# Kernel optimization log

Measured on AMD Instinct MI355X. Metric: run time of the kernel, lower is better.

Reference implementation:

```python
import jax, jax.numpy as jnp
import numpy as np

NUM_STRINGS = 6
WEIGHT_FRET_ONSET = 0.5
STRING_WEIGHTS = jnp.ones((NUM_STRINGS,), dtype=jnp.float32)

B, S, T, C = 64, 6, 2000, 25


def setup_inputs() -> dict:
    key = jax.random.key(0)
    k1, k2, k3, k4 = jax.random.split(key, 4)
    return {
        "output_fret": jax.random.normal(k1, (B, S, T, C), dtype=jnp.float32),
        "target_fret": jax.random.randint(k2, (B, S, T), 0, C),
        "output_onset": jax.random.normal(k3, (B, S, T), dtype=jnp.float32),
        "target_onset": jax.random.uniform(k4, (B, S, T), dtype=jnp.float32),
    }


def reference(output_fret, target_fret, output_onset, target_onset):
    # ---- fret loss: standard CE over classes, mean over batch per (s,t),
    #      summed over frames, weighted per string ----
    logp_fret = jax.nn.log_softmax(output_fret, axis=-1)            # [B,S,T,C]
    nll = -jnp.take_along_axis(logp_fret, target_fret[..., None], axis=-1)[..., 0]  # [B,S,T]
    fret_st = nll.mean(axis=0)                                       # [S,T] (reduction='mean' over batch)
    fret_string_losses = fret_st.sum(axis=1) * STRING_WEIGHTS        # [S]
    fret_loss = fret_string_losses.sum()

    # ---- onset loss: torch CE with 1D [B] input + [B] float target =
    #      single example with B classes and probability targets:
    #      softmax over the BATCH dimension ----
    logp_on = jax.nn.log_softmax(output_onset, axis=0)               # softmax over B
    on_st = -(target_onset * logp_on).sum(axis=0)                    # [S,T]
    onset_string_losses = on_st.sum(axis=1) * STRING_WEIGHTS         # [S]
    onset_loss = onset_string_losses.sum()

    loss = WEIGHT_FRET_ONSET * fret_loss + (1.0 - WEIGHT_FRET_ONSET) * onset_loss
    return (loss, fret_loss, onset_loss, fret_string_losses, onset_string_losses)
```

## Files before the change

kernel.cpp:

```cpp
#include <hip/hip_runtime.h>
#include <math.h>

constexpr int Bn = 64, Sn = 6, Tn = 2000, Cn = 25;
constexpr int COLS = Sn * Tn;
constexpr int ROWS = Bn * Sn * Tn;
constexpr int BDIM = 256;
constexpr int RPB  = 256;
constexpr int FBLK = ROWS / RPB;
constexpr int FPAD = 3072;
constexpr int OBLK = (COLS + BDIM - 1) / BDIM;
constexpr int OPAD = 64;
constexpr int GRID = FBLK + OBLK;


__global__ __launch_bounds__(BDIM) void main_kernel(const float4* __restrict__ x4,
                                                    const int*    __restrict__ tgt,
                                                    const float*  __restrict__ ox,
                                                    const float*  __restrict__ ot,
                                                    float* __restrict__ pf,
                                                    float* __restrict__ po) {
    __shared__ float lds[RPB * Cn];
    __shared__ float ls[Sn];
    const int tid = threadIdx.x;
    if (tid < Sn) ls[tid] = 0.0f;

    if (blockIdx.x < OBLK) {
        __syncthreads();
        const int col = blockIdx.x * BDIM + tid;
        if (col < COLS) {
            float M = -INFINITY, S = 0.0f, ts = 0.0f, txs = 0.0f;
            for (int b0 = 0; b0 < Bn; b0 += 16) {
                float xv[16];
                #pragma unroll
                for (int k = 0; k < 16; ++k) xv[k] = ox[(b0 + k) * COLS + col];
                #pragma unroll
                for (int k = 0; k < 16; ++k) {
                    const float tv = ot[(b0 + k) * COLS + col];
                    ts  += tv;
                    txs += tv * xv[k];
                }
                float cm = -INFINITY;
                #pragma unroll
                for (int k = 0; k < 16; ++k) cm = fmaxf(cm, xv[k]);
                float cs = 0.0f;
                #pragma unroll
                for (int k = 0; k < 16; ++k) cs += __expf(xv[k] - cm);
                const float nm = fmaxf(M, cm);
                S = S * __expf(M - nm) + cs * __expf(cm - nm);
                M = nm;
            }
            const float on = ts * (M + __logf(S)) - txs;
            atomicAdd(&ls[col / Tn], on);
        }
        __syncthreads();
        if (tid < Sn) po[tid * OPAD + blockIdx.x] = ls[tid];
    } else {
        const int fb = blockIdx.x - OBLK;
        const float4* src = x4 + (long)fb * (RPB * Cn / 4);
        float4* lds4 = (float4*)lds;
        #pragma unroll
        for (int k = tid; k < RPB * Cn / 4; k += BDIM) lds4[k] = src[k];
        __syncthreads();

        const int   row   = fb * RPB + tid;
        const float* myrow = lds + tid * Cn;
        float m = -INFINITY;
        #pragma unroll
        for (int c = 0; c < Cn; ++c) m = fmaxf(m, myrow[c]);
        float sum = 0.0f;
        #pragma unroll
        for (int c = 0; c < Cn; ++c) sum += __expf(myrow[c] - m);
        const float nll = m + __logf(sum) - myrow[tgt[row]];

        const int s = (row / Tn) % Sn;
        atomicAdd(&ls[s], nll);
        __syncthreads();
        if (tid < Sn) pf[tid * FPAD + fb] = ls[tid];
    }
}

__global__ __launch_bounds__(1024) void finish_kernel(const float* __restrict__ pf,
                                                      const float* __restrict__ po,
                                                      float* __restrict__ out) {
    __shared__ float acc[2 * Sn];
    const int tid  = threadIdx.x;
    const int lane = tid & 63;
    if (tid < 2 * Sn) acc[tid] = 0.0f;
    __syncthreads();

    float fs[Sn];
    #pragma unroll
    for (int s = 0; s < Sn; ++s) {
        float v = 0.0f;
        for (int i = tid; i < FBLK; i += 1024) v += pf[s * FPAD + i];
        fs[s] = v;
    }
    #pragma unroll
    for (int off = 32; off > 0; off >>= 1) {
        #pragma unroll
        for (int s = 0; s < Sn; ++s) fs[s] += __shfl_xor(fs[s], off, 64);
    }
    if (lane == 0) {
        #pragma unroll
        for (int s = 0; s < Sn; ++s) atomicAdd(&acc[s], fs[s]);
    }

    const int w = tid >> 6;
    if (w < Sn) {
        float v = (lane < OBLK) ? po[w * OPAD + lane] : 0.0f;
        #pragma unroll
        for (int off = 32; off > 0; off >>= 1) v += __shfl_xor(v, off, 64);
        if (lane == 0) acc[Sn + w] = v;
    }
    __syncthreads();

    if (tid == 0) {
        float fret = 0.0f, on = 0.0f, fsv[Sn], osv[Sn];
        #pragma unroll
        for (int s = 0; s < Sn; ++s) {
            fsv[s] = acc[s] * (1.0f / Bn);
            osv[s] = acc[Sn + s];
            fret += fsv[s];
            on   += osv[s];
        }
        out[0] = 0.5f * fret + 0.5f * on;
        out[1] = fret;
        out[2] = on;
        #pragma unroll
        for (int s = 0; s < Sn; ++s) { out[3 + s] = fsv[s]; out[9 + s] = osv[s]; }
    }
}

extern "C" void kernel_launch(void* const* d_in, const int* in_sizes, int n_in,
                              void* d_out, int out_size, void* d_ws, size_t ws_size,
                              hipStream_t stream) {
    const float* output_fret  = (const float*)d_in[0];
    const int*   target_fret  = (const int*)d_in[1];
    const float* output_onset = (const float*)d_in[2];
    const float* target_onset = (const float*)d_in[3];
    float* pf  = (float*)d_ws;
    float* po  = pf + Sn * FPAD;
    float* out = (float*)d_out;

    main_kernel<<<GRID, BDIM, 0, stream>>>((const float4*)output_fret, target_fret,
                                           output_onset, target_onset, pf, po);
    finish_kernel<<<1, 1024, 0, stream>>>(pf, po, out);
}
```

Baseline: 30.04 us.

## Fuse finish reduction into main kernel via last-block ticket, wave-level segmented reduce

```diff
diff --git a/kernel.cpp b/kernel.cpp
--- a/kernel.cpp
+++ b/kernel.cpp
@@ -12,22 +12,57 @@
 constexpr int OPAD = 64;
 constexpr int GRID = FBLK + OBLK;
 
+__device__ float    g_pf[Sn * FPAD];
+__device__ float    g_po[Sn * OPAD];
+__device__ unsigned g_ticket = 0;
+
+static __device__ __forceinline__ float agent_load(const float* p) {
+    return __hip_atomic_load(p, __ATOMIC_RELAXED, __HIP_MEMORY_SCOPE_AGENT);
+}
+static __device__ __forceinline__ void agent_store(float* p, float v) {
+    __hip_atomic_store(p, v, __ATOMIC_RELAXED, __HIP_MEMORY_SCOPE_AGENT);
+}
+
+static __device__ __forceinline__ void seg_reduce_add(float* ls, int s, float v, int lane) {
+    const int s0 = __shfl(s, 0, 64);
+    const int s1 = __shfl(s, 63, 64);
+    if (s0 == s1) {
+        float a = v;
+        #pragma unroll
+        for (int off = 32; off; off >>= 1) a += __shfl_xor(a, off, 64);
+        if (lane == 0) atomicAdd(&ls[s0], a);
+    } else {
+        float a = (s == s0) ? v : 0.0f;
+        float b = (s == s0) ? 0.0f : v;
+        #pragma unroll
+        for (int off = 32; off; off >>= 1) {
+            a += __shfl_xor(a, off, 64);
+            b += __shfl_xor(b, off, 64);
+        }
+        if (lane == 0) { atomicAdd(&ls[s0], a); atomicAdd(&ls[s1], b); }
+    }
+}
 
 __global__ __launch_bounds__(BDIM) void main_kernel(const float4* __restrict__ x4,
                                                     const int*    __restrict__ tgt,
                                                     const float*  __restrict__ ox,
                                                     const float*  __restrict__ ot,
-                                                    float* __restrict__ pf,
-                                                    float* __restrict__ po) {
+                                                    float* __restrict__ out) {
     __shared__ float lds[RPB * Cn];
     __shared__ float ls[Sn];
-    const int tid = threadIdx.x;
+    __shared__ float accf[Sn], acco[Sn];
+    __shared__ int   amLast;
+    const int tid  = threadIdx.x;
+    const int lane = tid & 63;
     if (tid < Sn) ls[tid] = 0.0f;
 
     if (blockIdx.x < OBLK) {
         __syncthreads();
         const int col = blockIdx.x * BDIM + tid;
+        float on = 0.0f;
+        int   s  = Sn - 1;
         if (col < COLS) {
+            s = col / Tn;
             float M = -INFINITY, S = 0.0f, ts = 0.0f, txs = 0.0f;
             for (int b0 = 0; b0 < Bn; b0 += 16) {
                 float xv[16];
@@ -49,20 +84,20 @@
                 S = S * __expf(M - nm) + cs * __expf(cm - nm);
                 M = nm;
             }
-            const float on = ts * (M + __logf(S)) - txs;
-            atomicAdd(&ls[col / Tn], on);
+            on = ts * (M + __logf(S)) - txs;
         }
+        seg_reduce_add(ls, s, on, lane);
         __syncthreads();
-        if (tid < Sn) po[tid * OPAD + blockIdx.x] = ls[tid];
+        if (tid < Sn) agent_store(&g_po[tid * OPAD + blockIdx.x], ls[tid]);
     } else {
-        const int fb = blockIdx.x - OBLK;
+        const int fb   = blockIdx.x - OBLK;
+        const int row  = fb * RPB + tid;
+        const int tcls = tgt[row];
         const float4* src = x4 + (long)fb * (RPB * Cn / 4);
         float4* lds4 = (float4*)lds;
-        #pragma unroll
         for (int k = tid; k < RPB * Cn / 4; k += BDIM) lds4[k] = src[k];
         __syncthreads();
 
-        const int   row   = fb * RPB + tid;
         const float* myrow = lds + tid * Cn;
         float m = -INFINITY;
         #pragma unroll
@@ -70,64 +105,64 @@
         float sum = 0.0f;
         #pragma unroll
         for (int c = 0; c < Cn; ++c) sum += __expf(myrow[c] - m);
-        const float nll = m + __logf(sum) - myrow[tgt[row]];
+        const float nll = m + __logf(sum) - myrow[tcls];
 
         const int s = (row / Tn) % Sn;
-        atomicAdd(&ls[s], nll);
+        seg_reduce_add(ls, s, nll, lane);
         __syncthreads();
-        if (tid < Sn) pf[tid * FPAD + fb] = ls[tid];
-    }
-}
-
-__global__ __launch_bounds__(1024) void finish_kernel(const float* __restrict__ pf,
-                                                      const float* __restrict__ po,
-                                                      float* __restrict__ out) {
-    __shared__ float acc[2 * Sn];
-    const int tid  = threadIdx.x;
-    const int lane = tid & 63;
-    if (tid < 2 * Sn) acc[tid] = 0.0f;
-    __syncthreads();
-
-    float fs[Sn];
-    #pragma unroll
-    for (int s = 0; s < Sn; ++s) {
-        float v = 0.0f;
-        for (int i = tid; i < FBLK; i += 1024) v += pf[s * FPAD + i];
-        fs[s] = v;
-    }
-    #pragma unroll
-    for (int off = 32; off > 0; off >>= 1) {
-        #pragma unroll
-        for (int s = 0; s < Sn; ++s) fs[s] += __shfl_xor(fs[s], off, 64);
-    }
-    if (lane == 0) {
-        #pragma unroll
-        for (int s = 0; s < Sn; ++s) atomicAdd(&acc[s], fs[s]);
+        if (tid < Sn) agent_store(&g_pf[tid * FPAD + fb], ls[tid]);
     }
 
-    const int w = tid >> 6;
-    if (w < Sn) {
-        float v = (lane < OBLK) ? po[w * OPAD + lane] : 0.0f;
-        #pragma unroll
-        for (int off = 32; off > 0; off >>= 1) v += __shfl_xor(v, off, 64);
-        if (lane == 0) acc[Sn + w] = v;
+    __syncthreads();
+    if (tid == 0) {
+        const unsigned old = __hip_atomic_fetch_add(&g_ticket, 1u, __ATOMIC_ACQ_REL,
+                                                    __HIP_MEMORY_SCOPE_AGENT);
+        amLast = ((old % (unsigned)GRID) == (unsigned)(GRID - 1)) ? 1 : 0;
     }
     __syncthreads();
-
-    if (tid == 0) {
-        float fret = 0.0f, on = 0.0f, fsv[Sn], osv[Sn];
+    if (amLast) {
+        if (tid < Sn) { accf[tid] = 0.0f; acco[tid] = 0.0f; }
+        __syncthreads();
+        float fs[Sn], os[Sn];
         #pragma unroll
         for (int s = 0; s < Sn; ++s) {
-            fsv[s] = acc[s] * (1.0f / Bn);
-            osv[s] = acc[Sn + s];
-            fret += fsv[s];
-            on   += osv[s];
+            float v = 0.0f;
+            for (int i = tid; i < FBLK; i += BDIM)
+                v += agent_load(&g_pf[s * FPAD + i]);
+            fs[s] = v;
+            float w = 0.0f;
+            for (int i = tid; i < OBLK; i += BDIM)
+                w += agent_load(&g_po[s * OPAD + i]);
+            os[s] = w;
         }
-        out[0] = 0.5f * fret + 0.5f * on;
-        out[1] = fret;
-        out[2] = on;
         #pragma unroll
-        for (int s = 0; s < Sn; ++s) { out[3 + s] = fsv[s]; out[9 + s] = osv[s]; }
+        for (int off = 32; off; off >>= 1) {
+            #pragma unroll
+            for (int s = 0; s < Sn; ++s) {
+                fs[s] += __shfl_xor(fs[s], off, 64);
+                os[s] += __shfl_xor(os[s], off, 64);
+            }
+        }
+        if (lane == 0) {
+            #pragma unroll
+            for (int s = 0; s < Sn; ++s) { atomicAdd(&accf[s], fs[s]); atomicAdd(&acco[s], os[s]); }
+        }
+        __syncthreads();
+        if (tid == 0) {
+            float fret = 0.0f, onv = 0.0f, fsv[Sn], osv[Sn];
+            #pragma unroll
+            for (int s = 0; s < Sn; ++s) {
+                fsv[s] = accf[s] * (1.0f / Bn);
+                osv[s] = acco[s];
+                fret += fsv[s];
+                onv  += osv[s];
+            }
+            out[0] = 0.5f * fret + 0.5f * onv;
+            out[1] = fret;
+            out[2] = onv;
+            #pragma unroll
+            for (int s = 0; s < Sn; ++s) { out[3 + s] = fsv[s]; out[9 + s] = osv[s]; }
+        }
     }
 }
 
@@ -138,11 +173,9 @@
     const int*   target_fret  = (const int*)d_in[1];
     const float* output_onset = (const float*)d_in[2];
     const float* target_onset = (const float*)d_in[3];
-    float* pf  = (float*)d_ws;
-    float* po  = pf + Sn * FPAD;
     float* out = (float*)d_out;
+    (void)d_ws; (void)ws_size;
 
     main_kernel<<<GRID, BDIM, 0, stream>>>((const float4*)output_fret, target_fret,
-                                           output_onset, target_onset, pf, po);
-    finish_kernel<<<1, 1024, 0, stream>>>(pf, po, out);
+                                           output_onset, target_onset, out);
 }
```

Result: slower. 102.6 us (+241.6%).

## Process fret rows directly from registers, vectorize onset columns, use wave-level reductions

Applied to the files above, without the earlier changes.

```diff
diff --git a/kernel.cpp b/kernel.cpp
--- a/kernel.cpp
+++ b/kernel.cpp
@@ -5,77 +5,130 @@
 constexpr int COLS = Sn * Tn;
 constexpr int ROWS = Bn * Sn * Tn;
 constexpr int BDIM = 256;
-constexpr int RPB  = 256;
+constexpr int WV   = BDIM / 64;
+
+constexpr int RPT  = 4;
+constexpr int RPB  = BDIM * RPT;
 constexpr int FBLK = ROWS / RPB;
-constexpr int FPAD = 3072;
-constexpr int OBLK = (COLS + BDIM - 1) / BDIM;
-constexpr int OPAD = 64;
-constexpr int GRID = FBLK + OBLK;
-
-
-__global__ __launch_bounds__(BDIM) void main_kernel(const float4* __restrict__ x4,
-                                                    const int*    __restrict__ tgt,
-                                                    const float*  __restrict__ ox,
-                                                    const float*  __restrict__ ot,
-                                                    float* __restrict__ pf,
-                                                    float* __restrict__ po) {
-    __shared__ float lds[RPB * Cn];
-    __shared__ float ls[Sn];
-    const int tid = threadIdx.x;
-    if (tid < Sn) ls[tid] = 0.0f;
+constexpr int FPAD = 768;
+
+constexpr int CPT  = 4;
+constexpr int CQN  = COLS / CPT;
+constexpr int OBLK = (CQN + BDIM - 1) / BDIM;
+constexpr int OPAD = 16;
+constexpr int GRID = OBLK + FBLK;
+
+static __device__ __forceinline__ float comp(const float4& v, int j) {
+    return j == 0 ? v.x : j == 1 ? v.y : j == 2 ? v.z : v.w;
+}
+
+static __device__ __forceinline__ void seg_reduce_add(float* ls, int s, float v, int lane) {
+    const int s0 = __shfl(s, 0, 64);
+    const int s1 = __shfl(s, 63, 64);
+    if (s0 == s1) {
+        float a = v;
+        #pragma unroll
+        for (int off = 32; off; off >>= 1) a += __shfl_xor(a, off, 64);
+        if (lane == 0) atomicAdd(&ls[s0], a);
+    } else {
+        float a = (s == s0) ? v : 0.0f;
+        float b = (s == s0) ? 0.0f : v;
+        #pragma unroll
+        for (int off = 32; off; off >>= 1) {
+            a += __shfl_xor(a, off, 64);
+            b += __shfl_xor(b, off, 64);
+        }
+        if (lane == 0) { atomicAdd(&ls[s0], a); atomicAdd(&ls[s1], b); }
+    }
+}
+
+__global__ __launch_bounds__(BDIM, 2) void main_kernel(const float4* __restrict__ x4,
+                                                       const int4*   __restrict__ tgt4,
+                                                       const float*  __restrict__ ox,
+                                                       const float*  __restrict__ ot,
+                                                       float* __restrict__ pf,
+                                                       float* __restrict__ po) {
+    __shared__ float ws[WV][Sn];
+    const int tid  = threadIdx.x;
+    const int lane = tid & 63;
+    const int w    = tid >> 6;
+    if (lane < Sn) ws[w][lane] = 0.0f;
 
     if (blockIdx.x < OBLK) {
+        const int cq = blockIdx.x * BDIM + tid;
+        float on = 0.0f;
+        int   s  = Sn - 1;
+        if (cq < CQN) {
+            s = (cq * CPT) / Tn;
+            const float4* oxp = (const float4*)ox + cq;
+            const float4* otp = (const float4*)ot + cq;
+            float M[4], S_[4], ts[4], txs[4];
+            #pragma unroll
+            for (int j = 0; j < 4; ++j) { M[j] = -INFINITY; S_[j] = 0.0f; ts[j] = 0.0f; txs[j] = 0.0f; }
+            for (int b0 = 0; b0 < Bn; b0 += 8) {
+                float4 xv[8], tv[8];
+                #pragma unroll
+                for (int k = 0; k < 8; ++k) xv[k] = oxp[(long)(b0 + k) * (COLS / 4)];
+                #pragma unroll
+                for (int k = 0; k < 8; ++k) tv[k] = otp[(long)(b0 + k) * (COLS / 4)];
+                #pragma unroll
+                for (int j = 0; j < 4; ++j) {
+                    float cm = -INFINITY;
+                    #pragma unroll
+                    for (int k = 0; k < 8; ++k) cm = fmaxf(cm, comp(xv[k], j));
+                    float cs = 0.0f;
+                    #pragma unroll
+                    for (int k = 0; k < 8; ++k) cs += __expf(comp(xv[k], j) - cm);
+                    const float nm = fmaxf(M[j], cm);
+                    S_[j] = S_[j] * __expf(M[j] - nm) + cs * __expf(cm - nm);
+                    M[j]  = nm;
+                    #pragma unroll
+                    for (int k = 0; k < 8; ++k) {
+                        const float t = comp(tv[k], j);
+                        ts[j]  += t;
+                        txs[j] += t * comp(xv[k], j);
+                    }
+                }
+            }
+            #pragma unroll
+            for (int j = 0; j < 4; ++j) on += ts[j] * (M[j] + __logf(S_[j])) - txs[j];
+        }
+        seg_reduce_add(ws[w], s, on, lane);
         __syncthreads();
-        const int col = blockIdx.x * BDIM + tid;
-        if (col < COLS) {
-            float M = -INFINITY, S = 0.0f, ts = 0.0f, txs = 0.0f;
-            for (int b0 = 0; b0 < Bn; b0 += 16) {
-                float xv[16];
-                #pragma unroll
-                for (int k = 0; k < 16; ++k) xv[k] = ox[(b0 + k) * COLS + col];
-                #pragma unroll
-                for (int k = 0; k < 16; ++k) {
-                    const float tv = ot[(b0 + k) * COLS + col];
-                    ts  += tv;
-                    txs += tv * xv[k];
-                }
-                float cm = -INFINITY;
-                #pragma unroll
-                for (int k = 0; k < 16; ++k) cm = fmaxf(cm, xv[k]);
-                float cs = 0.0f;
-                #pragma unroll
-                for (int k = 0; k < 16; ++k) cs += __expf(xv[k] - cm);
-                const float nm = fmaxf(M, cm);
-                S = S * __expf(M - nm) + cs * __expf(cm - nm);
-                M = nm;
+        if (tid < Sn)
+            po[tid * OPAD + blockIdx.x] = ws[0][tid] + ws[1][tid] + ws[2][tid] + ws[3][tid];
+    } else {
+        const int  fb = blockIdx.x - OBLK;
+        const long q  = (long)fb * BDIM + tid;
+        const float4* src = x4 + q * 25;
+        float v[RPT * Cn];
+        #pragma unroll
+        for (int c = 0; c < 25; ++c) {
+            const float4 t = src[c];
+            v[4 * c + 0] = t.x; v[4 * c + 1] = t.y; v[4 * c + 2] = t.z; v[4 * c + 3] = t.w;
+        }
+        const int4 t4 = tgt4[q];
+        float acc = 0.0f;
+        #pragma unroll
+        for (int r = 0; r < RPT; ++r) {
+            const int tc = (r == 0) ? t4.x : (r == 1) ? t4.y : (r == 2) ? t4.z : t4.w;
+            float m = -INFINITY, xt = 0.0f;
+            #pragma unroll
+            for (int c = 0; c < Cn; ++c) {
+                const float e = v[r * Cn + c];
+                m  = fmaxf(m, e);
+                xt = (c == tc) ? e : xt;
             }
-            const float on = ts * (M + __logf(S)) - txs;
-            atomicAdd(&ls[col / Tn], on);
-        }
+            float ssum = 0.0f;
+            #pragma unroll
+            for (int c = 0; c < Cn; ++c) ssum += __expf(v[r * Cn + c] - m);
+            acc += m + __logf(ssum) - xt;
+        }
+        const int s = (int)((q * RPT) / Tn) % Sn;
+        seg_reduce_add(ws[w], s, acc, lane);
         __syncthreads();
-        if (tid < Sn) po[tid * OPAD + blockIdx.x] = ls[tid];
-    } else {
-        const int fb = blockIdx.x - OBLK;
-        const float4* src = x4 + (long)fb * (RPB * Cn / 4);
-        float4* lds4 = (float4*)lds;
-        #pragma unroll
-        for (int k = tid; k < RPB * Cn / 4; k += BDIM) lds4[k] = src[k];
-        __syncthreads();
-
-        const int   row   = fb * RPB + tid;
-        const float* myrow = lds + tid * Cn;
-        float m = -INFINITY;
-        #pragma unroll
-        for (int c = 0; c < Cn; ++c) m = fmaxf(m, myrow[c]);
-        float sum = 0.0f;
-        #pragma unroll
-        for (int c = 0; c < Cn; ++c) sum += __expf(myrow[c] - m);
-        const float nll = m + __logf(sum) - myrow[tgt[row]];
-
-        const int s = (row / Tn) % Sn;
-        atomicAdd(&ls[s], nll);
-        __syncthreads();
-        if (tid < Sn) pf[tid * FPAD + fb] = ls[tid];
+        if (tid < Sn)
+            pf[tid * FPAD + fb] = ws[0][tid] + ws[1][tid] + ws[2][tid] + ws[3][tid];
     }
 }
 
@@ -96,7 +149,7 @@
         fs[s] = v;
     }
     #pragma unroll
-    for (int off = 32; off > 0; off >>= 1) {
+    for (int off = 32; off; off >>= 1) {
         #pragma unroll
         for (int s = 0; s < Sn; ++s) fs[s] += __shfl_xor(fs[s], off, 64);
     }
@@ -105,12 +158,12 @@
         for (int s = 0; s < Sn; ++s) atomicAdd(&acc[s], fs[s]);
     }
 
-    const int w = tid >> 6;
-    if (w < Sn) {
-        float v = (lane < OBLK) ? po[w * OPAD + lane] : 0.0f;
-        #pragma unroll
-        for (int off = 32; off > 0; off >>= 1) v += __shfl_xor(v, off, 64);
-        if (lane == 0) acc[Sn + w] = v;
+    const int wv = tid >> 6;
+    if (wv < Sn) {
+        float v = (lane < OBLK) ? po[wv * OPAD + lane] : 0.0f;
+        #pragma unroll
+        for (int off = 32; off; off >>= 1) v += __shfl_xor(v, off, 64);
+        if (lane == 0) acc[Sn + wv] = v;
     }
     __syncthreads();
 
@@ -142,7 +195,8 @@
     float* po  = pf + Sn * FPAD;
     float* out = (float*)d_out;
 
-    main_kernel<<<GRID, BDIM, 0, stream>>>((const float4*)output_fret, target_fret,
+    main_kernel<<<GRID, BDIM, 0, stream>>>((const float4*)output_fret,
+                                           (const int4*)target_fret,
                                            output_onset, target_onset, pf, po);
     finish_kernel<<<1, 1024, 0, stream>>>(pf, po, out);
 }
```

Result: slower. 33.30 us (+10.9%).
